# Kernel optimization log

Hardware: AMD Instinct MI355X
Metric: run time of the kernel (lower is better)

The kernel has to match this reference:

```python
import jax, jax.numpy as jnp
import numpy as np

B, K, D, DICT, C = 2048, 32, 768, 24576, 64


def setup_inputs() -> dict:
    key = jax.random.key(0)
    ks = jax.random.split(key, 9)
    up_vals = jax.random.uniform(ks[0], (B, K), dtype=jnp.float32)
    up_decoder_w = jax.random.normal(ks[1], (D, DICT), dtype=jnp.float32) * 0.02
    down_encoder_w = jax.random.normal(ks[2], (DICT, D), dtype=jnp.float32) * 0.02
    up_encoder_w = jax.random.normal(ks[3], (DICT, D), dtype=jnp.float32) * 0.02
    b_dec = jax.random.normal(ks[4], (D,), dtype=jnp.float32) * 0.02
    up_indices = jax.random.randint(ks[5], (B, K), 0, DICT)
    down_indices = jax.random.randint(ks[6], (B, K), 0, DICT)
    conn = jax.random.randint(ks[7], (DICT, C), 0, DICT)
    drop = jax.random.uniform(ks[8], (DICT, C)) < 0.1
    connections = jnp.where(drop, -1, conn)
    return {
        "up_vals": up_vals,
        "up_decoder_w": up_decoder_w,
        "down_encoder_w": down_encoder_w,
        "up_encoder_w": up_encoder_w,
        "b_dec": b_dec,
        "up_indices": up_indices,
        "down_indices": down_indices,
        "connections": connections,
    }


def reference(up_vals, up_decoder_w, down_encoder_w, up_encoder_w, b_dec,
              up_indices, down_indices, connections):
    # allowed upstream features per active downstream feature: [B, k_down, C]
    allowed = connections[down_indices]
    valid = allowed != -1
    # match[b,i,c,j] = allowed[b,i,c] == up_indices[b,j] (and slot valid)
    match = (allowed[..., None] == up_indices[:, None, None, :]) & valid[..., None]
    # multiplicity of each (down i, up j) pair across the C slots: [B, k_down, k_up]
    mult = match.sum(axis=2).astype(up_vals.dtype)
    # gather active decoder/encoder vectors
    act_up = up_decoder_w.T[up_indices]          # [B, k_up, D]
    act_down = down_encoder_w[down_indices]      # [B, k_down, D]
    # virtual weights between active down and up features
    vw = jnp.einsum('bid,bjd->bij', act_down, act_up)  # [B, k_down, k_up]
    contributions = jnp.einsum('bij,bij->bi', vw, mult * up_vals[:, None, :])
    # bias contribution (note: indexed by up_indices, broadcast add as in source)
    b_dec_contrib = up_encoder_w @ b_dec         # [DICT]
    return contributions + b_dec_contrib[up_indices]
```

## Files before the change

### kernel.cpp

```cpp
#include <hip/hip_runtime.h>

#define B_    2048
#define K_    32
#define D_    768
#define DICT_ 24576
#define C_    64

#define CCHUNK   512
#define DCHUNK   16
#define NCC      (DICT_ / CCHUNK)
#define NDC      (D_ / DCHUNK)
#define BCAP     2048

#define REC_F 0
#define BDC_F (NCC * BCAP * 4)
#define CNT_F (BDC_F + DICT_)
#define WS_FLOATS (CNT_F + NCC * 16)

__global__ void bdc_kernel(const float* __restrict__ up_enc,
                           const float* __restrict__ b_dec,
                           float* __restrict__ bdc,
                           int* __restrict__ cnt) {
    if (blockIdx.x == 0 && threadIdx.x < NCC) cnt[threadIdx.x * 16] = 0;
    int wave = threadIdx.x >> 6;
    int lane = threadIdx.x & 63;
    int row  = blockIdx.x * 4 + wave;
    const float4* rp = (const float4*)(up_enc + (size_t)row * D_);
    const float4* bp = (const float4*)b_dec;
    float acc = 0.f;
    #pragma unroll
    for (int i = 0; i < 3; ++i) {
        float4 a = rp[lane + 64 * i];
        float4 b = bp[lane + 64 * i];
        acc += a.x * b.x + a.y * b.y + a.z * b.z + a.w * b.w;
    }
    #pragma unroll
    for (int off = 32; off; off >>= 1) acc += __shfl_xor(acc, off);
    if (lane == 0) bdc[row] = acc;
}

__global__ void scan_kernel(const float* __restrict__ up_vals,
                            const float* __restrict__ bdc,
                            const int*   __restrict__ up_idx,
                            const int*   __restrict__ down_idx,
                            const int*   __restrict__ conn,
                            int*  __restrict__ cnt,
                            int4* __restrict__ recs,
                            float* __restrict__ out) {
    int wave = threadIdx.x >> 6;
    int lane = threadIdx.x & 63;
    int item = blockIdx.x * 4 + wave;
    int b    = item >> 5;

    int di = down_idx[item];
    int allowed = conn[(size_t)di * C_ + lane];
    bool valid = allowed >= 0;
    int   myup  = up_idx[b * K_ + (lane & 31)];
    float myval = up_vals[b * K_ + (lane & 31)];

    if (lane == 0) out[item] = bdc[up_idx[item]];

    unsigned jm = 0u;
    #pragma unroll
    for (int j = 0; j < K_; ++j) {
        int tgt = __builtin_amdgcn_readlane(myup, j);
        jm |= (valid && (allowed == tgt)) ? (1u << j) : 0u;
    }

    if (__ballot(jm != 0u)) {
        #pragma unroll 1
        for (int j = 0; j < K_; ++j) {
            unsigned long long m = __ballot((jm >> j) & 1u);
            if (m != 0) {
                int   t = __shfl(myup, j);
                float w = (float)__popcll(m) * __shfl(myval, j);
                if (lane == 0) {
                    int bi  = t >> 9;
                    int pos = atomicAdd(cnt + bi * 16, 1);
                    if (pos < BCAP)
                        recs[bi * BCAP + pos] = make_int4(item, di, __float_as_int(w), t);
                }
            }
        }
    }
}

__global__ __launch_bounds__(256) void pair_dot_kernel(const float* __restrict__ A,
                                                       const float* __restrict__ down_enc,
                                                       const int*  __restrict__ cnt,
                                                       const int4* __restrict__ recs,
                                                       float* __restrict__ out) {
    __shared__ float tile[DCHUNK * CCHUNK];
    int tid = threadIdx.x;
    int cc = blockIdx.x, dc = blockIdx.y;
    int c0 = cc * CCHUNK, d0 = dc * DCHUNK;

    int n = cnt[cc * 16];
    if (n > BCAP) n = BCAP;
    if (n == 0) return;

    #pragma unroll
    for (int k = 0; k < 8; ++k) {
        int l  = tid + 256 * k;
        int r  = l >> 7, fi = l & 127;
        ((float4*)tile)[l] = *(const float4*)(A + (size_t)(d0 + r) * DICT_ + c0 + 4 * fi);
    }
    __syncthreads();

    const int4* bucket = recs + (size_t)cc * BCAP;
    for (int i = tid; i < n; i += 256) {
        int4 rec = bucket[i];
        int t = rec.w - c0;
        const float4* dp = (const float4*)(down_enc + (size_t)rec.y * D_ + d0);
        float acc = 0.f;
        #pragma unroll
        for (int q = 0; q < 4; ++q) {
            float4 dv = dp[q];
            acc += dv.x * tile[(4 * q + 0) * CCHUNK + t]
                 + dv.y * tile[(4 * q + 1) * CCHUNK + t]
                 + dv.z * tile[(4 * q + 2) * CCHUNK + t]
                 + dv.w * tile[(4 * q + 3) * CCHUNK + t];
        }
        atomicAdd(out + rec.x, __int_as_float(rec.z) * acc);
    }
}

__global__ void main_fallback(const float* __restrict__ up_vals,
                              const float* __restrict__ up_dec,
                              const float* __restrict__ down_enc,
                              const float* __restrict__ up_enc,
                              const float* __restrict__ b_dec,
                              const int*   __restrict__ up_idx,
                              const int*   __restrict__ down_idx,
                              const int*   __restrict__ conn,
                              float* __restrict__ out) {
    int wave = threadIdx.x >> 6;
    int lane = threadIdx.x & 63;
    int item = blockIdx.x * 4 + wave;
    int b    = item >> 5;

    int di = down_idx[item];
    int allowed = conn[(size_t)di * C_ + lane];
    bool valid = allowed >= 0;
    int   myup  = up_idx[b * K_ + (lane & 31)];
    float myval = up_vals[b * K_ + (lane & 31)];

    unsigned jm = 0u;
    #pragma unroll
    for (int j = 0; j < K_; ++j) {
        int tgt = __builtin_amdgcn_readlane(myup, j);
        jm |= (valid && (allowed == tgt)) ? (1u << j) : 0u;
    }

    float acc = 0.f;
    if (__ballot(jm != 0u)) {
        const float* drow = down_enc + (size_t)di * D_;
        #pragma unroll 1
        for (int j = 0; j < K_; ++j) {
            unsigned long long m = __ballot((jm >> j) & 1u);
            if (m != 0) {
                float w   = (float)__popcll(m) * __shfl(myval, j);
                int   tgt = __shfl(myup, j);
                const float* colp = up_dec + tgt;
                float partial = 0.f;
                #pragma unroll
                for (int ii = 0; ii < 12; ++ii) {
                    int d = lane + 64 * ii;
                    partial += drow[d] * colp[(size_t)d * DICT_];
                }
                acc += w * partial;
            }
        }
    }

    {
        int ui = up_idx[item];
        const float4* rp = (const float4*)(up_enc + (size_t)ui * D_);
        const float4* bp = (const float4*)b_dec;
        #pragma unroll
        for (int ii = 0; ii < 3; ++ii) {
            float4 a  = rp[lane + 64 * ii];
            float4 bb = bp[lane + 64 * ii];
            acc += a.x * bb.x + a.y * bb.y + a.z * bb.z + a.w * bb.w;
        }
    }

    #pragma unroll
    for (int off = 32; off; off >>= 1) acc += __shfl_xor(acc, off);
    if (lane == 0) out[item] = acc;
}

extern "C" void kernel_launch(void* const* d_in, const int* in_sizes, int n_in,
                              void* d_out, int out_size, void* d_ws, size_t ws_size,
                              hipStream_t stream) {
    (void)in_sizes; (void)n_in; (void)out_size;
    const float* up_vals  = (const float*)d_in[0];
    const float* up_dec   = (const float*)d_in[1];
    const float* down_enc = (const float*)d_in[2];
    const float* up_enc   = (const float*)d_in[3];
    const float* b_dec    = (const float*)d_in[4];
    const int*   up_idx   = (const int*)d_in[5];
    const int*   down_idx = (const int*)d_in[6];
    const int*   conn     = (const int*)d_in[7];
    float* out = (float*)d_out;

    if (ws_size < (size_t)WS_FLOATS * sizeof(float)) {
        main_fallback<<<(B_ * K_) / 4, 256, 0, stream>>>(up_vals, up_dec, down_enc,
                                                         up_enc, b_dec, up_idx,
                                                         down_idx, conn, out);
        return;
    }

    float* ws   = (float*)d_ws;
    int4*  recs = (int4*)(ws + REC_F);
    float* bdc  = ws + BDC_F;
    int*   cnt  = (int*)(ws + CNT_F);

    bdc_kernel<<<DICT_ / 4, 256, 0, stream>>>(up_enc, b_dec, bdc, cnt);
    scan_kernel<<<(B_ * K_) / 4, 256, 0, stream>>>(up_vals, bdc, up_idx, down_idx,
                                                   conn, cnt, recs, out);
    pair_dot_kernel<<<dim3(NCC, NDC), 256, 0, stream>>>(up_dec, down_enc, cnt,
                                                        recs, out);
}
```

Before: 240.6 us.

## Fuse bias-dot computation into scan kernel and add final merge pass

Folds the per-dictionary-row bias dot product into the scan kernel, so the first few waves of each batch row compute four bdc rows each. This removes the dependency that made the scan wait for a separate bdc kernel. Partial contributions now accumulate into a workspace buffer, and a new merge kernel adds the gathered bias at the end. It trades one launch for a memset and a small extra elementwise kernel, and the scan kernel's waves become uneven in work.

```diff
diff --git a/kernel.cpp b/kernel.cpp
--- a/kernel.cpp
+++ b/kernel.cpp
@@ -11,42 +11,24 @@
 #define NCC      (DICT_ / CCHUNK)
 #define NDC      (D_ / DCHUNK)
 #define BCAP     2048
+#define NITEMS   (B_ * K_)
 
 #define REC_F 0
 #define BDC_F (NCC * BCAP * 4)
 #define CNT_F (BDC_F + DICT_)
-#define WS_FLOATS (CNT_F + NCC * 16)
-
-__global__ void bdc_kernel(const float* __restrict__ up_enc,
-                           const float* __restrict__ b_dec,
-                           float* __restrict__ bdc,
-                           int* __restrict__ cnt) {
-    if (blockIdx.x == 0 && threadIdx.x < NCC) cnt[threadIdx.x * 16] = 0;
-    int wave = threadIdx.x >> 6;
-    int lane = threadIdx.x & 63;
-    int row  = blockIdx.x * 4 + wave;
-    const float4* rp = (const float4*)(up_enc + (size_t)row * D_);
-    const float4* bp = (const float4*)b_dec;
-    float acc = 0.f;
-    #pragma unroll
-    for (int i = 0; i < 3; ++i) {
-        float4 a = rp[lane + 64 * i];
-        float4 b = bp[lane + 64 * i];
-        acc += a.x * b.x + a.y * b.y + a.z * b.z + a.w * b.w;
-    }
-    #pragma unroll
-    for (int off = 32; off; off >>= 1) acc += __shfl_xor(acc, off);
-    if (lane == 0) bdc[row] = acc;
-}
-
-__global__ void scan_kernel(const float* __restrict__ up_vals,
-                            const float* __restrict__ bdc,
-                            const int*   __restrict__ up_idx,
-                            const int*   __restrict__ down_idx,
-                            const int*   __restrict__ conn,
-                            int*  __restrict__ cnt,
-                            int4* __restrict__ recs,
-                            float* __restrict__ out) {
+#define ACC_F (CNT_F + NCC * 16)
+#define WS_FLOATS (ACC_F + NITEMS)
+
+__global__ void fused_scan_bdc(const float* __restrict__ up_vals,
+                               const float* __restrict__ up_enc,
+                               const float* __restrict__ b_dec,
+                               const int*   __restrict__ up_idx,
+                               const int*   __restrict__ down_idx,
+                               const int*   __restrict__ conn,
+                               int*   __restrict__ cnt,
+                               int4*  __restrict__ recs,
+                               float* __restrict__ bdc,
+                               float* __restrict__ acc) {
     int wave = threadIdx.x >> 6;
     int lane = threadIdx.x & 63;
     int item = blockIdx.x * 4 + wave;
@@ -58,7 +40,7 @@
     int   myup  = up_idx[b * K_ + (lane & 31)];
     float myval = up_vals[b * K_ + (lane & 31)];
 
-    if (lane == 0) out[item] = bdc[up_idx[item]];
+    if (lane == 0) acc[item] = 0.f;
 
     unsigned jm = 0u;
     #pragma unroll
@@ -83,13 +65,33 @@
             }
         }
     }
+
+    if ((item & 31) < 3) {
+        int quad = (item >> 5) * 3 + (item & 31);
+        const float4* bp = (const float4*)b_dec;
+        #pragma unroll
+        for (int rr = 0; rr < 4; ++rr) {
+            int row = quad * 4 + rr;
+            const float4* rp = (const float4*)(up_enc + (size_t)row * D_);
+            float a2 = 0.f;
+            #pragma unroll
+            for (int i = 0; i < 3; ++i) {
+                float4 a  = rp[lane + 64 * i];
+                float4 bb = bp[lane + 64 * i];
+                a2 += a.x * bb.x + a.y * bb.y + a.z * bb.z + a.w * bb.w;
+            }
+            #pragma unroll
+            for (int off = 32; off; off >>= 1) a2 += __shfl_xor(a2, off);
+            if (lane == 0) bdc[row] = a2;
+        }
+    }
 }
 
 __global__ __launch_bounds__(256) void pair_dot_kernel(const float* __restrict__ A,
                                                        const float* __restrict__ down_enc,
                                                        const int*  __restrict__ cnt,
                                                        const int4* __restrict__ recs,
-                                                       float* __restrict__ out) {
+                                                       float* __restrict__ acc) {
     __shared__ float tile[DCHUNK * CCHUNK];
     int tid = threadIdx.x;
     int cc = blockIdx.x, dc = blockIdx.y;
@@ -112,17 +114,25 @@
         int4 rec = bucket[i];
         int t = rec.w - c0;
         const float4* dp = (const float4*)(down_enc + (size_t)rec.y * D_ + d0);
-        float acc = 0.f;
+        float a2 = 0.f;
         #pragma unroll
         for (int q = 0; q < 4; ++q) {
             float4 dv = dp[q];
-            acc += dv.x * tile[(4 * q + 0) * CCHUNK + t]
-                 + dv.y * tile[(4 * q + 1) * CCHUNK + t]
-                 + dv.z * tile[(4 * q + 2) * CCHUNK + t]
-                 + dv.w * tile[(4 * q + 3) * CCHUNK + t];
-        }
-        atomicAdd(out + rec.x, __int_as_float(rec.z) * acc);
-    }
+            a2 += dv.x * tile[(4 * q + 0) * CCHUNK + t]
+                + dv.y * tile[(4 * q + 1) * CCHUNK + t]
+                + dv.z * tile[(4 * q + 2) * CCHUNK + t]
+                + dv.w * tile[(4 * q + 3) * CCHUNK + t];
+        }
+        atomicAdd(acc + rec.x, __int_as_float(rec.z) * a2);
+    }
+}
+
+__global__ void merge_kernel(const float* __restrict__ bdc,
+                             const float* __restrict__ acc,
+                             const int*   __restrict__ up_idx,
+                             float* __restrict__ out) {
+    int i = blockIdx.x * 256 + threadIdx.x;
+    out[i] = bdc[up_idx[i]] + acc[i];
 }
 
 __global__ void main_fallback(const float* __restrict__ up_vals,
@@ -215,10 +225,12 @@
     int4*  recs = (int4*)(ws + REC_F);
     float* bdc  = ws + BDC_F;
     int*   cnt  = (int*)(ws + CNT_F);
-
-    bdc_kernel<<<DICT_ / 4, 256, 0, stream>>>(up_enc, b_dec, bdc, cnt);
-    scan_kernel<<<(B_ * K_) / 4, 256, 0, stream>>>(up_vals, bdc, up_idx, down_idx,
-                                                   conn, cnt, recs, out);
+    float* acc  = ws + ACC_F;
+
+    hipMemsetAsync(cnt, 0, (size_t)NCC * 16 * sizeof(int), stream);
+    fused_scan_bdc<<<NITEMS / 4, 256, 0, stream>>>(up_vals, up_enc, b_dec, up_idx,
+                                                   down_idx, conn, cnt, recs, bdc, acc);
     pair_dot_kernel<<<dim3(NCC, NDC), 256, 0, stream>>>(up_dec, down_enc, cnt,
-                                                        recs, out);
-}
+                                                        recs, acc);
+    merge_kernel<<<NITEMS / 256, 256, 0, stream>>>(bdc, acc, up_idx, out);
+}
```

Result: slower. 268.3 us (+11.5%).
